# Performance work log

Hardware: AMD Instinct MI355X
Metric: run time of the kernel (lower is better)

Reference implementation:

```python
import jax, jax.numpy as jnp
import numpy as np

TOPK = 10000          # config.test_layer_topk
CLASS_NUM = 1         # config.num_classes - 1
LEVEL_SIZES = [98304, 24576, 6144, 1536, 384]
NUM_GT = 2000


def _rand_boxes(key, n):
    k1, k2, k3, k4 = jax.random.split(key, 4)
    x1 = jax.random.uniform(k1, (n,)) * 1600.0
    y1 = jax.random.uniform(k2, (n,)) * 900.0
    w = jax.random.uniform(k3, (n,)) * 192.0 + 8.0
    h = jax.random.uniform(k4, (n,)) * 192.0 + 8.0
    return jnp.stack([x1, y1, x1 + w, y1 + h], axis=1).astype(jnp.float32)


def setup_inputs() -> dict:
    key = jax.random.key(0)
    keys = jax.random.split(key, 32)
    inp = {}
    for i, n in enumerate(LEVEL_SIZES):
        inp[f"anchors{i}"] = _rand_boxes(keys[i], n)
        # raw logits biased negative like a trained RetinaNet cls head
        inp[f"cls{i}"] = (jax.random.normal(keys[8 + i], (1, n, CLASS_NUM)) - 4.0).astype(jnp.float32)
        inp[f"reg{i}"] = (jax.random.normal(keys[16 + i], (1, n, 8)) * 0.2).astype(jnp.float32)
    gb = _rand_boxes(keys[24], NUM_GT)
    inp["gt_boxes"] = jnp.concatenate([gb, jnp.ones((NUM_GT, 1), jnp.float32)], axis=1)[None]
    inp["num_gt"] = NUM_GT
    return inp


def _bbox_transform_inv(rois, deltas):
    # CrowdDet convention: width = x2 - x1 + 1
    w = rois[:, 2] - rois[:, 0] + 1.0
    h = rois[:, 3] - rois[:, 1] + 1.0
    cx = rois[:, 0] + 0.5 * w
    cy = rois[:, 1] + 0.5 * h
    pcx = deltas[:, 0] * w + cx
    pcy = deltas[:, 1] * h + cy
    pw = jnp.exp(deltas[:, 2]) * w
    ph = jnp.exp(deltas[:, 3]) * h
    return jnp.stack([pcx - 0.5 * pw, pcy - 0.5 * ph,
                      pcx + 0.5 * pw - 1.0, pcy + 0.5 * ph - 1.0], axis=1)


def _bbox_transform(rois, gt):
    w = rois[:, 2] - rois[:, 0] + 1.0
    h = rois[:, 3] - rois[:, 1] + 1.0
    cx = rois[:, 0] + 0.5 * w
    cy = rois[:, 1] + 0.5 * h
    gw = gt[:, 2] - gt[:, 0] + 1.0
    gh = gt[:, 3] - gt[:, 1] + 1.0
    gcx = gt[:, 0] + 0.5 * gw
    gcy = gt[:, 1] + 0.5 * gh
    return jnp.stack([(gcx - cx) / w, (gcy - cy) / h,
                      jnp.log(gw / w), jnp.log(gh / h)], axis=1)


def _box_overlap(a, b):
    # pairwise IoU [Na, Nb], +1 area convention
    area_a = (a[:, 2] - a[:, 0] + 1.0) * (a[:, 3] - a[:, 1] + 1.0)
    area_b = (b[:, 2] - b[:, 0] + 1.0) * (b[:, 3] - b[:, 1] + 1.0)
    iw = jnp.clip(jnp.minimum(a[:, None, 2], b[None, :, 2]) -
                  jnp.maximum(a[:, None, 0], b[None, :, 0]) + 1.0, 0.0)
    ih = jnp.clip(jnp.minimum(a[:, None, 3], b[None, :, 3]) -
                  jnp.maximum(a[:, None, 1], b[None, :, 1]) + 1.0, 0.0)
    inter = iw * ih
    return inter / (area_a[:, None] + area_b[None, :] - inter)


def _forward(anchors_list, cls_list, reg_list, gt_boxes, num_gt):
    keep_anchors, keep_cls, keep_reg, keep_lstd = [], [], [], []
    for anchors, pcls, preg in zip(anchors_list, cls_list, reg_list):
        anchors = anchors.reshape(-1, 4)
        cls = pcls[0].reshape(-1, CLASS_NUM)
        reg8 = preg[0].reshape(-1, 8)
        reg, lstd = reg8[:, :4], reg8[:, 4:]
        n = anchors.shape[0]
        if n > TOPK:
            ruler = jnp.max(cls, axis=1)
            _, inds = jax.lax.top_k(ruler, TOPK)
            keep_anchors.append(anchors[inds])
            keep_cls.append(jax.nn.sigmoid(cls[inds]))
            keep_reg.append(reg[inds])
            keep_lstd.append(lstd[inds])
        else:
            keep_anchors.append(anchors)
            keep_cls.append(jax.nn.sigmoid(cls))
            keep_reg.append(reg)
            keep_lstd.append(lstd)
    keep_anchors = jnp.concatenate(keep_anchors, axis=0)   # [N,4]
    keep_cls = jnp.concatenate(keep_cls, axis=0)            # [N,C]
    keep_reg = jnp.concatenate(keep_reg, axis=0)            # [N,4]

    N = keep_cls.shape[0]
    tag = jnp.tile(jnp.arange(CLASS_NUM, dtype=keep_cls.dtype) + 1.0, (N, 1)).reshape(-1, 1)
    pred_scores = keep_cls.reshape(-1, 1)
    pred_bbox = _bbox_transform_inv(keep_anchors, keep_reg)            # [N,4]
    pred_bbox = jnp.tile(pred_bbox, (1, CLASS_NUM)).reshape(-1, 4)     # [N*C,4]

    pred_gtboxes = gt_boxes[0, :num_gt, :4]                            # [G,4]
    pred_iou = _box_overlap(pred_bbox, pred_gtboxes)                   # [N*C,G]
    gt_assignment = jnp.argmax(pred_iou, axis=1)                       # topk(1)
    assigned_gt = pred_gtboxes[gt_assignment]                          # [N*C,4]
    keep_target = _bbox_transform(keep_anchors, assigned_gt)           # [N,4] (C=1)

    pred_bbox6 = jnp.concatenate([pred_bbox, pred_scores, tag], axis=1)  # [N*C,6]
    return jnp.concatenate([pred_bbox6, keep_target], axis=1)            # [N,10]


def reference(anchors0, anchors1, anchors2, anchors3, anchors4,
              cls0, cls1, cls2, cls3, cls4,
              reg0, reg1, reg2, reg3, reg4,
              gt_boxes, num_gt):
    return _forward([anchors0, anchors1, anchors2, anchors3, anchors4],
                    [cls0, cls1, cls2, cls3, cls4],
                    [reg0, reg1, reg2, reg3, reg4],
                    gt_boxes, num_gt)
```

## Files before the change

kernel.cpp:

```cpp
#include <hip/hip_runtime.h>
#include <stdint.h>

#define K_TOP 10000
#define N0    98304
#define N1    24576
#define N2    6144
#define N3    1536
#define N4    384
#define NSMALL (N2 + N3 + N4)
#define BMAX0  192
#define BMAX1  320
#define D0     18432
#define D1     15360
#define JSPLIT 32
#define JC0    576
#define JC1    480
#define PART1  ((size_t)JSPLIT * D0)
#define SLOTS  (D0 + D1 + NSMALL)
#define MAXGT 2048
#define LUTW   8.0f
#define LUTN   256

struct Ptrs { const float* anc[5]; const float* cls[5]; const float* reg[5]; };

__device__ __forceinline__ unsigned f2ord(float f) {
    unsigned u = __float_as_uint(f);
    return (u & 0x80000000u) ? ~u : (u | 0x80000000u);
}

__global__ void __launch_bounds__(512)
k_front(const float* __restrict__ cls0, const float* __restrict__ cls1,
        unsigned long long* __restrict__ cand,
        const float* __restrict__ gt, const int* __restrict__ numgt,
        float4* __restrict__ sbox, unsigned short* __restrict__ sidxG,
        unsigned* __restrict__ lutG, float* __restrict__ maxwG) {
    unsigned tid = threadIdx.x, wave = tid >> 6, lane = tid & 63u;
    int bi = (int)blockIdx.x;

    if (bi < 144) {
        int lev = (bi < 96) ? 0 : 1;
        int bx  = (bi < 96) ? bi : bi - 96;
        const float* cls = lev ? cls1 : cls0;
        const float4* s4 = (const float4*)cls;
        unsigned nq4     = lev ? 3072u : 4096u;
        unsigned targetS = lev ? 5900u : 1966u;

        __shared__ unsigned h[8][256];
        __shared__ unsigned sfx[256];
        __shared__ unsigned sd[2];
        __shared__ unsigned lcnt;

        for (unsigned i = tid; i < 2048u; i += 512u) ((unsigned*)h)[i] = 0;
        __syncthreads();
        for (unsigned q = tid; q < nq4; q += 512u) {
            float4 v = s4[q];
            atomicAdd(&h[wave][f2ord(v.x) >> 24], 1u);
            atomicAdd(&h[wave][f2ord(v.y) >> 24], 1u);
            atomicAdd(&h[wave][f2ord(v.z) >> 24], 1u);
            atomicAdd(&h[wave][f2ord(v.w) >> 24], 1u);
        }
        __syncthreads();
        if (tid < 256) {
            unsigned s = 0;
            #pragma unroll
            for (int w = 0; w < 8; w++) s += h[w][tid];
            sfx[tid] = s;
        }
        __syncthreads();
        for (int off = 1; off < 256; off <<= 1) {
            unsigned v = 0;
            if (tid < 256) v = sfx[tid] + ((tid + off < 256) ? sfx[tid + off] : 0u);
            __syncthreads();
            if (tid < 256) sfx[tid] = v;
            __syncthreads();
        }
        if (tid < 256) {
            unsigned suf = sfx[tid];
            unsigned sufN = (tid < 255) ? sfx[tid + 1] : 0u;
            if (suf >= targetS && sufN < targetS) { sd[0] = tid; sd[1] = targetS - sufN; }
        }
        for (unsigned i = tid; i < 2048u; i += 512u) ((unsigned*)h)[i] = 0;
        __syncthreads();
        unsigned tb = sd[0], remS = sd[1];
        for (unsigned q = tid; q < nq4; q += 512u) {
            float4 v = s4[q];
            unsigned k0 = f2ord(v.x), k1 = f2ord(v.y), k2 = f2ord(v.z), k3 = f2ord(v.w);
            if ((k0 >> 24) == tb) atomicAdd(&h[wave][(k0 >> 16) & 255u], 1u);
            if ((k1 >> 24) == tb) atomicAdd(&h[wave][(k1 >> 16) & 255u], 1u);
            if ((k2 >> 24) == tb) atomicAdd(&h[wave][(k2 >> 16) & 255u], 1u);
            if ((k3 >> 24) == tb) atomicAdd(&h[wave][(k3 >> 16) & 255u], 1u);
        }
        __syncthreads();
        if (tid < 256) {
            unsigned s = 0;
            #pragma unroll
            for (int w = 0; w < 8; w++) s += h[w][tid];
            sfx[tid] = s;
        }
        __syncthreads();
        for (int off = 1; off < 256; off <<= 1) {
            unsigned v = 0;
            if (tid < 256) v = sfx[tid] + ((tid + off < 256) ? sfx[tid + off] : 0u);
            __syncthreads();
            if (tid < 256) sfx[tid] = v;
            __syncthreads();
        }
        if (tid < 256) {
            unsigned suf = sfx[tid];
            unsigned sufN = (tid < 255) ? sfx[tid + 1] : 0u;
            if (suf >= remS && sufN < remS) sd[0] = tid;
        }
        if (tid == 0) lcnt = 0;
        __syncthreads();
        unsigned T = ((tb << 8) | sd[0]) << 16;

        unsigned n = lev ? (unsigned)N1 : (unsigned)N0;
        unsigned bmax = lev ? BMAX1 : BMAX0;
        unsigned iters = lev ? 1u : 2u;
        unsigned long long l0 = 0, l1 = 0;
        unsigned c = 0;
        unsigned i = (unsigned)bx * 512u + tid;
        for (unsigned t = 0; t < iters; t++, i += 96u * 512u) {
            if (i < n) {
                unsigned key = f2ord(cls[i]);
                if (key >= T) {
                    unsigned long long v = ((unsigned long long)key << 32) | (unsigned)(~i);
                    if (c == 0) l0 = v; else l1 = v;
                    c++;
                }
            }
        }
        unsigned ls = 0;
        if (c) ls = atomicAdd(&lcnt, c);
        __syncthreads();
        unsigned long long* cl = cand + (lev ? (size_t)D0 : 0) + (size_t)bx * bmax;
        if (c > 0 && ls + 0 < bmax) cl[ls + 0] = l0;
        if (c > 1 && ls + 1 < bmax) cl[ls + 1] = l1;
        for (unsigned s2 = lcnt + tid; s2 < bmax; s2 += 512u) cl[s2] = 0ull;
    } else if (bi < 176) {
        __shared__ __align__(16) unsigned keys[MAXGT];
        __shared__ unsigned prank[8][64];
        int ng = *numgt; if (ng > MAXGT) ng = MAXGT;
        for (int j = (int)tid; j < MAXGT; j += 512)
            keys[j] = (j < ng) ? f2ord(gt[(size_t)j * 5 + 0]) : 0xFFFFFFFFu;
        __syncthreads();
        int i = (bi - 144) * 64 + (int)lane;
        unsigned ki = (i < ng) ? keys[i] : 0xFFFFFFFFu;
        unsigned rank = 0;
        const uint4* k4 = (const uint4*)(keys + wave * 256u);
        #pragma unroll 8
        for (int q = 0; q < 64; q++) {
            uint4 kv = k4[q];
            int j = (int)(wave * 256u) + q * 4;
            rank += (kv.x < ki || (kv.x == ki && j + 0 < i)) ? 1u : 0u;
            rank += (kv.y < ki || (kv.y == ki && j + 1 < i)) ? 1u : 0u;
            rank += (kv.z < ki || (kv.z == ki && j + 2 < i)) ? 1u : 0u;
            rank += (kv.w < ki || (kv.w == ki && j + 3 < i)) ? 1u : 0u;
        }
        prank[wave][lane] = rank;
        __syncthreads();
        if (tid < 64) {
            int ii = (bi - 144) * 64 + (int)tid;
            if (ii < ng) {
                unsigned r = 0;
                #pragma unroll
                for (int w2 = 0; w2 < 8; w2++) r += prank[w2][tid];
                float x1 = gt[(size_t)ii * 5 + 0], y1 = gt[(size_t)ii * 5 + 1];
                float x2 = gt[(size_t)ii * 5 + 2], y2 = gt[(size_t)ii * 5 + 3];
                sbox[r]  = make_float4(x1, y1, x2 + 1.0f, y2 + 1.0f);
                sidxG[r] = (unsigned short)ii;
            }
        }
    } else {
        __shared__ unsigned hb[LUTN];
        __shared__ unsigned sc[LUTN];
        __shared__ float wm[8];
        int ng = *numgt; if (ng > MAXGT) ng = MAXGT;
        for (unsigned i = tid; i < LUTN; i += 512u) hb[i] = 0;
        __syncthreads();
        float w = 0.f;
        for (int j = (int)tid; j < ng; j += 512) {
            float x1 = gt[(size_t)j * 5 + 0];
            float x2 = gt[(size_t)j * 5 + 2];
            w = fmaxf(w, x2 - x1 + 1.0f);
            int b = (int)(x1 * (1.0f / LUTW));
            if (b < 0) b = 0; if (b > LUTN - 1) b = LUTN - 1;
            atomicAdd(&hb[b], 1u);
        }
        #pragma unroll
        for (int off = 32; off >= 1; off >>= 1) w = fmaxf(w, __shfl_xor(w, off));
        if (lane == 0) wm[wave] = w;
        __syncthreads();
        if (tid < LUTN) sc[tid] = hb[tid];
        __syncthreads();
        for (int off = 1; off < LUTN; off <<= 1) {
            unsigned v = 0;
            if (tid < LUTN) v = sc[tid] + ((int)tid - off >= 0 ? sc[tid - off] : 0u);
            __syncthreads();
            if (tid < LUTN) sc[tid] = v;
            __syncthreads();
        }
        if (tid < LUTN) lutG[tid] = (tid == 0) ? 0u : sc[tid - 1];
        if (tid == 0) {
            lutG[LUTN] = (unsigned)ng;
            float m = wm[0];
            #pragma unroll
            for (int k = 1; k < 8; k++) m = fmaxf(m, wm[k]);
            *maxwG = m;
        }
    }
}

__global__ void __launch_bounds__(512)
k_rank(const unsigned long long* __restrict__ cand, unsigned short* __restrict__ part) {
    unsigned tid = threadIdx.x;
    int bi = (int)blockIdx.x;
    int lev = (bi < 384) ? 0 : 1;
    int idx = (bi < 384) ? bi : bi - 384;
    unsigned ic = (unsigned)(idx >> 5), jc = (unsigned)(idx & 31);
    unsigned D   = lev ? D1 : D0;
    unsigned jch = lev ? JC1 : JC0;
    const unsigned long long* cl = cand + (lev ? (size_t)D0 : 0);
    unsigned ibase = ic * 1536u;
    unsigned long long ci0 = cl[ibase + tid];
    unsigned long long ci1 = cl[ibase + tid + 512u];
    unsigned long long ci2 = cl[ibase + tid + 1024u];
    unsigned j0 = jc * jch;
    unsigned lim2 = jch >> 1;
    __shared__ __align__(16) unsigned long long tile[JC0];
    if (tid < lim2)
        ((ulonglong2*)tile)[tid] = ((const ulonglong2*)(cl + j0))[tid];
    __syncthreads();
    unsigned rk0 = 0, rk1 = 0, rk2 = 0;
    const ulonglong2* t2 = (const ulonglong2*)tile;
    #pragma unroll 4
    for (unsigned t = 0; t < lim2; t++) {
        ulonglong2 cj = t2[t];
        rk0 += (cj.x > ci0) ? 1u : 0u; rk0 += (cj.y > ci0) ? 1u : 0u;
        rk1 += (cj.x > ci1) ? 1u : 0u; rk1 += (cj.y > ci1) ? 1u : 0u;
        rk2 += (cj.x > ci2) ? 1u : 0u; rk2 += (cj.y > ci2) ? 1u : 0u;
    }
    unsigned short* pp = part + (lev ? PART1 : 0) + (size_t)jc * D + ibase + tid;
    pp[0]    = (unsigned short)rk0;
    pp[512]  = (unsigned short)rk1;
    pp[1024] = (unsigned short)rk2;
}

__global__ void __launch_bounds__(512)
k_iou(Ptrs p, const unsigned long long* __restrict__ cand,
      const unsigned short* __restrict__ part,
      const float4* __restrict__ sbox, const unsigned short* __restrict__ sidxG,
      const unsigned* __restrict__ lutG, const float* __restrict__ maxwG,
      const float* __restrict__ gt, const int* __restrict__ numgt,
      float* __restrict__ out) {
    __shared__ float4 sg[MAXGT];
    __shared__ unsigned short sgi[MAXGT];
    __shared__ unsigned slut[LUTN + 1];
    int ng = *numgt; if (ng > MAXGT) ng = MAXGT;
    unsigned tid = threadIdx.x;
    for (int j = (int)tid; j < ng; j += 512) { sg[j] = sbox[j]; sgi[j] = sidxG[j]; }
    for (unsigned j = tid; j <= LUTN; j += 512u) slut[j] = lutG[j];
    float maxw = *maxwG;
    __syncthreads();

    unsigned wave = tid >> 6;
    int lane = (int)(tid & 63u);
    unsigned sbase = ((unsigned)blockIdx.x * 8u + wave) * 4u;

    int valid = 0, row = 0;
    float bx1 = 0.f, by1 = 0.f, bx2 = 0.f, by2 = 0.f;
    float dw = 1.f, dh = 1.f, dcx = 0.f, dcy = 0.f;
    if (lane < 4) {
        unsigned s = sbase + (unsigned)lane;
        int lev = 0, ai = 0;
        if (s < (unsigned)(D0 + D1)) {
            lev = (s >= (unsigned)D0) ? 1 : 0;
            unsigned i = lev ? (s - D0) : s;
            unsigned long long v = cand[(lev ? (size_t)D0 : 0) + i];
            if (v != 0ull) {
                unsigned D = lev ? D1 : D0;
                const unsigned short* pp = part + (lev ? PART1 : 0) + i;
                unsigned rank = 0;
                #pragma unroll
                for (int j = 0; j < JSPLIT; j++)
                    rank += pp[(size_t)j * D];
                if (rank < K_TOP) {
                    valid = 1;
                    row = lev * K_TOP + (int)rank;
                    ai = (int)~(unsigned)v;
                }
            }
        } else {
            int rr = (int)s - (D0 + D1);
            row = 2 * K_TOP + rr; valid = 1;
            if (rr < N2)           { lev = 2; ai = rr; }
            else if (rr < N2 + N3) { lev = 3; ai = rr - N2; }
            else                   { lev = 4; ai = rr - N2 - N3; }
        }
        if (valid) {
            float4 a4 = ((const float4*)p.anc[lev])[ai];
            float sc = p.cls[lev][ai];
            float4 r4 = *(const float4*)(p.reg[lev] + (size_t)ai * 8);
            dw = a4.z - a4.x + 1.0f;  dh = a4.w - a4.y + 1.0f;
            dcx = a4.x + 0.5f * dw;   dcy = a4.y + 0.5f * dh;
            float pcx = r4.x * dw + dcx, pcy = r4.y * dh + dcy;
            float pw = expf(r4.z) * dw,  ph = expf(r4.w) * dh;
            bx1 = pcx - 0.5f * pw;    by1 = pcy - 0.5f * ph;
            bx2 = pcx + 0.5f * pw - 1.0f;
            by2 = pcy + 0.5f * ph - 1.0f;
            float* o = out + (size_t)row * 10;
            o[0] = bx1; o[1] = by1; o[2] = bx2; o[3] = by2;
            o[4] = 1.0f / (1.0f + expf(-sc));
            o[5] = 1.0f;
        }
    }

    #pragma unroll
    for (int k = 0; k < 4; k++) {
        int vk = __shfl(valid, k, 64);
        if (!vk) continue;
        float kx1 = __shfl(bx1, k, 64), ky1 = __shfl(by1, k, 64);
        float kx2 = __shfl(bx2, k, 64), ky2 = __shfl(by2, k, 64);
        float A = (kx2 - kx1 + 1.0f) * (ky2 - ky1 + 1.0f);
        float x2p = kx2 + 1.0f, y2p = ky2 + 1.0f;
        float vlo = kx1 - maxw - 1.0f;
        float vhi = kx2 + 2.0f;
        int blo = (vlo <= 0.f) ? 0 : (int)(vlo * (1.0f / LUTW));
        if (blo > LUTN - 1) blo = LUTN - 1;
        int bhi = (vhi <= 0.f) ? 0 : ((int)(vhi * (1.0f / LUTW)) + 1);
        if (bhi > LUTN) bhi = LUTN;
        int lo = (int)slut[blo], hi = (int)slut[bhi];

        float I = 0.f, S = 1.f;
        int arg = (lane == 0) ? 0 : 0x7FFFFFFF;
        for (int t = lo + lane; t < hi; t += 64) {
            float4 gb = sg[t];
            float iw = fminf(x2p, gb.z) - fmaxf(kx1, gb.x); iw = fmaxf(iw, 0.f);
            float ih = fminf(y2p, gb.w) - fmaxf(ky1, gb.y); ih = fmaxf(ih, 0.f);
            float Ii = iw * ih;
            float Ss = A + (gb.z - gb.x) * (gb.w - gb.y);
            float xs = Ii * S, ys = I * Ss;
            int gi = (int)sgi[t];
            if (xs > ys || (xs == ys && gi < arg)) { I = Ii; S = Ss; arg = gi; }
        }
        #pragma unroll
        for (int off = 1; off < 64; off <<= 1) {
            float oI = __shfl_xor(I, off), oS = __shfl_xor(S, off);
            int   oa = __shfl_xor(arg, off);
            float x = oI * S, y = I * oS;
            if (x > y || (x == y && oa < arg)) { I = oI; S = oS; arg = oa; }
        }
        if (lane == k) {
            if (arg >= ng) arg = 0;
            const float* gb = gt + (size_t)arg * 5;
            float gx1 = gb[0], gy1 = gb[1], gx2 = gb[2], gy2 = gb[3];
            float gw = gx2 - gx1 + 1.0f, gh = gy2 - gy1 + 1.0f;
            float gcx = gx1 + 0.5f * gw,  gcy = gy1 + 0.5f * gh;
            float* o = out + (size_t)row * 10;
            o[6] = (gcx - dcx) / dw;
            o[7] = (gcy - dcy) / dh;
            o[8] = logf(gw / dw);
            o[9] = logf(gh / dh);
        }
    }
}

extern "C" void kernel_launch(void* const* d_in, const int* in_sizes, int n_in,
                              void* d_out, int out_size, void* d_ws, size_t ws_size,
                              hipStream_t stream) {
    Ptrs p;
    bool interleaved = (in_sizes[2] == N0 * 8);
    for (int l = 0; l < 5; l++) {
        if (interleaved) {
            p.anc[l] = (const float*)d_in[3 * l + 0];
            p.cls[l] = (const float*)d_in[3 * l + 1];
            p.reg[l] = (const float*)d_in[3 * l + 2];
        } else {
            p.anc[l] = (const float*)d_in[l];
            p.cls[l] = (const float*)d_in[5 + l];
            p.reg[l] = (const float*)d_in[10 + l];
        }
    }
    const float* gt    = (const float*)d_in[15];
    const int*   numgt = (const int*)d_in[16];

    char* ws = (char*)d_ws;
    size_t off = 0;
    unsigned long long* cand = (unsigned long long*)(ws + off);  off += (size_t)(D0 + D1) * 8;
    unsigned short* part = (unsigned short*)(ws + off);          off += (size_t)JSPLIT * (D0 + D1) * 2;
    float4* sbox = (float4*)(ws + off);                          off += (size_t)MAXGT * 16;
    unsigned short* sidxG = (unsigned short*)(ws + off);         off += (size_t)MAXGT * 2;
    unsigned* lutG = (unsigned*)(ws + off);                      off += (size_t)(LUTN + 4) * 4;
    float* maxwG = (float*)(ws + off);                           off += 256;

    float* out = (float*)d_out;

    k_front<<<dim3(177), dim3(512), 0, stream>>>(p.cls[0], p.cls[1], cand,
                                                 gt, numgt, sbox, sidxG, lutG, maxwG);
    k_rank<<<dim3(704), dim3(512), 0, stream>>>(cand, part);
    k_iou<<<dim3(SLOTS / 32), dim3(512), 0, stream>>>(p, cand, part, sbox, sidxG,
                                                      lutG, maxwG, gt, numgt, out);
}
```

Before: 94.86 us.

## Compact candidates into global per-level lists via atomic counters and size rank grid

Candidate keys are no longer written into fixed padded per-block slots. They are appended to a compact per-level list using a global atomic counter. The rank kernel reads the actual count, sizes its j-chunks to it, and skips blocks past the count, so it does less pairwise comparison work on empty slots. This adds a memset of the counters and candidate buffer, plus global atomics. Candidate order now depends on atomic ordering, but ranks are still computed by full comparison.

```diff
diff --git a/kernel.cpp b/kernel.cpp
--- a/kernel.cpp
+++ b/kernel.cpp
@@ -8,15 +8,10 @@
 #define N3    1536
 #define N4    384
 #define NSMALL (N2 + N3 + N4)
-#define BMAX0  192
-#define BMAX1  320
-#define D0     18432
-#define D1     15360
+#define ICAP   16896
 #define JSPLIT 32
-#define JC0    576
-#define JC1    480
-#define PART1  ((size_t)JSPLIT * D0)
-#define SLOTS  (D0 + D1 + NSMALL)
+#define PARTL  ((size_t)JSPLIT * ICAP)
+#define SLOTS  (2 * ICAP + NSMALL)
 #define MAXGT 2048
 #define LUTW   8.0f
 #define LUTN   256
@@ -30,7 +25,7 @@
 
 __global__ void __launch_bounds__(512)
 k_front(const float* __restrict__ cls0, const float* __restrict__ cls1,
-        unsigned long long* __restrict__ cand,
+        unsigned* __restrict__ cntG, unsigned long long* __restrict__ cand,
         const float* __restrict__ gt, const int* __restrict__ numgt,
         float4* __restrict__ sbox, unsigned short* __restrict__ sidxG,
         unsigned* __restrict__ lutG, float* __restrict__ maxwG) {
@@ -48,7 +43,7 @@
         __shared__ unsigned h[8][256];
         __shared__ unsigned sfx[256];
         __shared__ unsigned sd[2];
-        __shared__ unsigned lcnt;
+        __shared__ unsigned lcnt, gbase;
 
         for (unsigned i = tid; i < 2048u; i += 512u) ((unsigned*)h)[i] = 0;
         __syncthreads();
@@ -115,7 +110,6 @@
         unsigned T = ((tb << 8) | sd[0]) << 16;
 
         unsigned n = lev ? (unsigned)N1 : (unsigned)N0;
-        unsigned bmax = lev ? BMAX1 : BMAX0;
         unsigned iters = lev ? 1u : 2u;
         unsigned long long l0 = 0, l1 = 0;
         unsigned c = 0;
@@ -133,10 +127,12 @@
         unsigned ls = 0;
         if (c) ls = atomicAdd(&lcnt, c);
         __syncthreads();
-        unsigned long long* cl = cand + (lev ? (size_t)D0 : 0) + (size_t)bx * bmax;
-        if (c > 0 && ls + 0 < bmax) cl[ls + 0] = l0;
-        if (c > 1 && ls + 1 < bmax) cl[ls + 1] = l1;
-        for (unsigned s2 = lcnt + tid; s2 < bmax; s2 += 512u) cl[s2] = 0ull;
+        if (tid == 0) gbase = lcnt ? atomicAdd(&cntG[lev], lcnt) : 0u;
+        __syncthreads();
+        unsigned b = gbase + ls;
+        unsigned long long* cl = cand + (size_t)lev * ICAP;
+        if (c > 0 && b + 0 < ICAP) cl[b + 0] = l0;
+        if (c > 1 && b + 1 < ICAP) cl[b + 1] = l1;
     } else if (bi < 176) {
         __shared__ __align__(16) unsigned keys[MAXGT];
         __shared__ unsigned prank[8][64];
@@ -212,22 +208,25 @@
 }
 
 __global__ void __launch_bounds__(512)
-k_rank(const unsigned long long* __restrict__ cand, unsigned short* __restrict__ part) {
+k_rank(const unsigned long long* __restrict__ cand, const unsigned* __restrict__ cntG,
+       unsigned short* __restrict__ part) {
     unsigned tid = threadIdx.x;
     int bi = (int)blockIdx.x;
-    int lev = (bi < 384) ? 0 : 1;
-    int idx = (bi < 384) ? bi : bi - 384;
+    int lev = (bi < 352) ? 0 : 1;
+    int idx = (bi < 352) ? bi : bi - 352;
     unsigned ic = (unsigned)(idx >> 5), jc = (unsigned)(idx & 31);
-    unsigned D   = lev ? D1 : D0;
-    unsigned jch = lev ? JC1 : JC0;
-    const unsigned long long* cl = cand + (lev ? (size_t)D0 : 0);
+    unsigned cnt = cntG[lev]; if (cnt > ICAP) cnt = ICAP;
+    unsigned cntP = (cnt + 63u) & ~63u;
     unsigned ibase = ic * 1536u;
+    if (ibase >= cntP) return;
+    const unsigned long long* cl = cand + (size_t)lev * ICAP;
     unsigned long long ci0 = cl[ibase + tid];
     unsigned long long ci1 = cl[ibase + tid + 512u];
     unsigned long long ci2 = cl[ibase + tid + 1024u];
+    unsigned jch = cntP >> 5;
     unsigned j0 = jc * jch;
     unsigned lim2 = jch >> 1;
-    __shared__ __align__(16) unsigned long long tile[JC0];
+    __shared__ __align__(16) unsigned long long tile[544];
     if (tid < lim2)
         ((ulonglong2*)tile)[tid] = ((const ulonglong2*)(cl + j0))[tid];
     __syncthreads();
@@ -240,7 +239,7 @@
         rk1 += (cj.x > ci1) ? 1u : 0u; rk1 += (cj.y > ci1) ? 1u : 0u;
         rk2 += (cj.x > ci2) ? 1u : 0u; rk2 += (cj.y > ci2) ? 1u : 0u;
     }
-    unsigned short* pp = part + (lev ? PART1 : 0) + (size_t)jc * D + ibase + tid;
+    unsigned short* pp = part + (lev ? PARTL : 0) + (size_t)jc * ICAP + ibase + tid;
     pp[0]    = (unsigned short)rk0;
     pp[512]  = (unsigned short)rk1;
     pp[1024] = (unsigned short)rk2;
@@ -273,17 +272,16 @@
     if (lane < 4) {
         unsigned s = sbase + (unsigned)lane;
         int lev = 0, ai = 0;
-        if (s < (unsigned)(D0 + D1)) {
-            lev = (s >= (unsigned)D0) ? 1 : 0;
-            unsigned i = lev ? (s - D0) : s;
-            unsigned long long v = cand[(lev ? (size_t)D0 : 0) + i];
+        if (s < 2u * ICAP) {
+            lev = (s >= (unsigned)ICAP) ? 1 : 0;
+            unsigned i = lev ? (s - ICAP) : s;
+            unsigned long long v = cand[(size_t)lev * ICAP + i];
             if (v != 0ull) {
-                unsigned D = lev ? D1 : D0;
-                const unsigned short* pp = part + (lev ? PART1 : 0) + i;
+                const unsigned short* pp = part + (lev ? PARTL : 0) + i;
                 unsigned rank = 0;
                 #pragma unroll
                 for (int j = 0; j < JSPLIT; j++)
-                    rank += pp[(size_t)j * D];
+                    rank += pp[(size_t)j * ICAP];
                 if (rank < K_TOP) {
                     valid = 1;
                     row = lev * K_TOP + (int)rank;
@@ -291,7 +289,7 @@
                 }
             }
         } else {
-            int rr = (int)s - (D0 + D1);
+            int rr = (int)s - 2 * ICAP;
             row = 2 * K_TOP + rr; valid = 1;
             if (rr < N2)           { lev = 2; ai = rr; }
             else if (rr < N2 + N3) { lev = 3; ai = rr - N2; }
@@ -386,8 +384,9 @@
 
     char* ws = (char*)d_ws;
     size_t off = 0;
-    unsigned long long* cand = (unsigned long long*)(ws + off);  off += (size_t)(D0 + D1) * 8;
-    unsigned short* part = (unsigned short*)(ws + off);          off += (size_t)JSPLIT * (D0 + D1) * 2;
+    unsigned* cntG = (unsigned*)(ws + off);                      off += 256;
+    unsigned long long* cand = (unsigned long long*)(ws + off);  off += (size_t)2 * ICAP * 8;
+    unsigned short* part = (unsigned short*)(ws + off);          off += (size_t)JSPLIT * 2 * ICAP * 2;
     float4* sbox = (float4*)(ws + off);                          off += (size_t)MAXGT * 16;
     unsigned short* sidxG = (unsigned short*)(ws + off);         off += (size_t)MAXGT * 2;
     unsigned* lutG = (unsigned*)(ws + off);                      off += (size_t)(LUTN + 4) * 4;
@@ -395,9 +394,10 @@
 
     float* out = (float*)d_out;
 
-    k_front<<<dim3(177), dim3(512), 0, stream>>>(p.cls[0], p.cls[1], cand,
+    hipMemsetAsync(d_ws, 0, 256 + (size_t)2 * ICAP * 8, stream);
+    k_front<<<dim3(177), dim3(512), 0, stream>>>(p.cls[0], p.cls[1], cntG, cand,
                                                  gt, numgt, sbox, sidxG, lutG, maxwG);
-    k_rank<<<dim3(704), dim3(512), 0, stream>>>(cand, part);
+    k_rank<<<dim3(704), dim3(512), 0, stream>>>(cand, cntG, part);
     k_iou<<<dim3(SLOTS / 32), dim3(512), 0, stream>>>(p, cand, part, sbox, sidxG,
                                                       lutG, maxwG, gt, numgt, out);
 }
```

Result: faster. 79.81 us (-15.9%).
